# Optimization experiments

Hardware: AMD Instinct MI355X
Metric: run time of the kernel (lower is better)

The kernel has to match this reference:

```python
import jax, jax.numpy as jnp
import numpy as np

TOP_K = 8
NUM_EXPERTS = 64
TEMPERATURE = 1.0
ALPHA = 0.01
EPS = 1e-20


def setup_inputs() -> dict:
    key = jax.random.key(0)
    k1, k2 = jax.random.split(key)
    hidden_states = jax.random.normal(k1, (4, 8192, 1024), dtype=jnp.float32)
    # kaiming_uniform-ish scale for the router weight
    bound = 1.0 / np.sqrt(1024.0)
    weight = jax.random.uniform(k2, (NUM_EXPERTS, 1024), dtype=jnp.float32,
                                minval=-bound, maxval=bound)
    return {"hidden_states": hidden_states, "weight": weight}


def reference(hidden_states, weight):
    bsz, seq_len, hidden_dim = hidden_states.shape
    flat = hidden_states.reshape(-1, hidden_dim)            # [N, H], N = bsz*seq_len
    logits = jnp.einsum('nh,eh->ne', flat, weight) / TEMPERATURE  # [N, E]
    scores = jax.nn.softmax(logits, axis=-1)                # [N, E]
    topk_weight, topk_idx = jax.lax.top_k(scores, TOP_K)    # [N, k] each
    # renormalize top-k probabilities
    topk_weight = topk_weight / (topk_weight.sum(axis=-1, keepdims=True) + EPS)
    # aux load-balancing loss (seq_aux=False branch), scores detached
    scores_aux = jax.lax.stop_gradient(scores)
    idx_flat = topk_idx.reshape(-1)                         # [N*k]
    ce = jnp.zeros((NUM_EXPERTS,), dtype=jnp.float32).at[idx_flat].add(1.0)
    ce = ce / idx_flat.shape[0]                             # mean of one-hot rows
    pi = scores_aux.mean(axis=0)                            # [E]
    fi = ce * NUM_EXPERTS
    aux_loss = (pi * fi).sum() * ALPHA
    return topk_idx, topk_weight, aux_loss
```

## Files before the change

### kernel.cpp

```cpp
#include <hip/hip_runtime.h>

#define H 1024
#define E 64
#define BT 64
#define THETA 2e-4f

typedef __attribute__((ext_vector_type(4))) float f4;
typedef __attribute__((ext_vector_type(16))) float f32x16;
typedef __bf16 bf16x8 __attribute__((ext_vector_type(8)));
typedef unsigned int u32;
typedef __attribute__((ext_vector_type(4))) u32 u32x4;

__device__ __forceinline__ u32 cvtpk_bf16(float a, float b) {
    u32 r;
    asm("v_cvt_pk_bf16_f32 %0, %1, %2" : "=v"(r) : "v"(a), "v"(b));
    return r;
}
__device__ __forceinline__ float asfloat(u32 u) { union { u32 u; float f; } c; c.u = u; return c.f; }

__device__ __forceinline__ void split8(f4 a, f4 b, u32x4& hi, u32x4& lo) {
    float x0[4] = {a.x, a.z, b.x, b.z};
    float x1[4] = {a.y, a.w, b.y, b.w};
    #pragma unroll
    for (int i = 0; i < 4; ++i) {
        u32 h = cvtpk_bf16(x0[i], x1[i]);
        float r0 = x0[i] - asfloat(h << 16);
        float r1 = x1[i] - asfloat(h & 0xFFFF0000u);
        hi[i] = h;
        lo[i] = cvtpk_bf16(r0, r1);
    }
}

__device__ __forceinline__ void async16(const void* g, void* l) {
    __builtin_amdgcn_global_load_lds(
        (const __attribute__((address_space(1))) unsigned int*)g,
        (__attribute__((address_space(3))) unsigned int*)l,
        16, 0, 0);
}

__global__ __launch_bounds__(512, 4)
void gate_main(const float* __restrict__ hs, const float* __restrict__ wt,
               float* __restrict__ out, float* __restrict__ pi_ws,
               float* __restrict__ ce_ws, unsigned int* __restrict__ risk_cnt,
               unsigned int* __restrict__ risk_list, unsigned int risk_cap,
               int n_tokens) {
    __shared__ float smem[16384];
    const int t = threadIdx.x;
    const int wave = t >> 6, lane = t & 63;
    const int tok_base = blockIdx.x * BT;
    char* sb = (char*)smem;

    const int srow = t >> 3;
    const int srcj = (t & 7) ^ (srow & 7);
    const float* gA = hs + (size_t)(tok_base + srow) * H + srcj * 4;
    const float* gB = wt + (size_t)srow * H + srcj * 4;
    const int sdest = wave << 10;

    const int lr = lane & 31, kh = lane >> 5;
    const int q4 = wave & 3, kh2 = wave >> 2;
    const int wrow = (q4 >> 1) * 32;
    const int wcol = (q4 & 1) * 32;
    const int arow = wrow + lr, brow = wcol + lr;
    const int s0 = kh2 * 4 + kh * 2;
    const int aoff = arow * 128 + ((s0 ^ (arow & 7)) << 4);
    const int boff = 8192 + brow * 128 + ((s0 ^ (brow & 7)) << 4);

    f32x16 acc0, acc1;
    #pragma unroll
    for (int i = 0; i < 16; ++i) { acc0[i] = 0.f; acc1[i] = 0.f; }

    auto stage = [&](int c) {
        char* bb = sb + (c & 3) * 16384;
        async16(gA + c * 32, bb + sdest);
        async16(gB + c * 32, bb + 8192 + sdest);
    };
    auto compute = [&](int c) {
        const char* cb = sb + (c & 3) * 16384;
        f4 a0 = *(const f4*)(cb + aoff);
        f4 a1 = *(const f4*)(cb + (aoff ^ 16));
        f4 b0 = *(const f4*)(cb + boff);
        f4 b1 = *(const f4*)(cb + (boff ^ 16));
        u32x4 ahp, alp, bhp, blp;
        split8(a0, a1, ahp, alp);
        split8(b0, b1, bhp, blp);
        const bf16x8 ah = __builtin_bit_cast(bf16x8, ahp);
        const bf16x8 al = __builtin_bit_cast(bf16x8, alp);
        const bf16x8 bh = __builtin_bit_cast(bf16x8, bhp);
        const bf16x8 bl = __builtin_bit_cast(bf16x8, blp);
        acc0 = __builtin_amdgcn_mfma_f32_32x32x16_bf16(ah, bh, acc0, 0, 0, 0);
        acc1 = __builtin_amdgcn_mfma_f32_32x32x16_bf16(ah, bl, acc1, 0, 0, 0);
        acc1 = __builtin_amdgcn_mfma_f32_32x32x16_bf16(al, bh, acc1, 0, 0, 0);
    };

    stage(0); stage(1); stage(2);
    for (int c = 0; c < 30; ++c) {
        asm volatile("s_waitcnt vmcnt(4)" ::: "memory");
        __builtin_amdgcn_s_barrier();
        __builtin_amdgcn_sched_barrier(0);
        if (c < 29) stage(c + 3);
        __builtin_amdgcn_sched_barrier(0);
        compute(c);
    }
    asm volatile("s_waitcnt vmcnt(2)" ::: "memory");
    __builtin_amdgcn_s_barrier();
    __builtin_amdgcn_sched_barrier(0);
    compute(30);
    asm volatile("s_waitcnt vmcnt(0)" ::: "memory");
    __builtin_amdgcn_s_barrier();
    __builtin_amdgcn_sched_barrier(0);
    compute(31);
    __syncthreads();

    float* S = smem;
    f4* S4 = (f4*)smem;
    float* P2    = smem + 4352;
    float* recip = smem + 8448;
    float* hist  = smem + 8512;
    float* pi7   = smem + 8576;

    {
        float vs[16];
        #pragma unroll
        for (int i = 0; i < 16; ++i) vs[i] = acc0[i] + acc1[i];
        if (kh2) {
            #pragma unroll
            for (int gq = 0; gq < 4; ++gq)
                #pragma unroll
                for (int qq = 0; qq < 4; ++qq)
                    P2[q4 * 1024 + (qq + gq * 8 + kh * 4) * 32 + lr] = vs[gq * 4 + qq];
        }
        if (t < 64) hist[t] = 0.f;
        __syncthreads();
        if (!kh2) {
            #pragma unroll
            for (int gq = 0; gq < 4; ++gq)
                #pragma unroll
                for (int qq = 0; qq < 4; ++qq) {
                    const int row = qq + gq * 8 + kh * 4;
                    S[(wrow + row) * 68 + wcol + lr] =
                        vs[gq * 4 + qq] + P2[q4 * 1024 + row * 32 + lr];
                }
        }
    }
    __syncthreads();

    if (t < 256) {
        const int tok = t >> 2, q = t & 3;
        f4 v[4];
        #pragma unroll
        for (int c2 = 0; c2 < 4; ++c2) v[c2] = S4[tok * 17 + q * 4 + c2];
        float m = v[0].x;
        #pragma unroll
        for (int c2 = 0; c2 < 4; ++c2)
            m = fmaxf(m, fmaxf(fmaxf(v[c2].x, v[c2].y), fmaxf(v[c2].z, v[c2].w)));
        m = fmaxf(m, __shfl_xor(m, 1, 64));
        m = fmaxf(m, __shfl_xor(m, 2, 64));
        float lsum = 0.f;
        #pragma unroll
        for (int c2 = 0; c2 < 4; ++c2) {
            v[c2].x = __expf(v[c2].x - m); v[c2].y = __expf(v[c2].y - m);
            v[c2].z = __expf(v[c2].z - m); v[c2].w = __expf(v[c2].w - m);
            lsum += (v[c2].x + v[c2].y) + (v[c2].z + v[c2].w);
        }
        #pragma unroll
        for (int c2 = 0; c2 < 4; ++c2) S4[tok * 17 + q * 4 + c2] = v[c2];
        lsum += __shfl_xor(lsum, 1, 64);
        lsum += __shfl_xor(lsum, 2, 64);
        if (q == 0) recip[tok] = 1.0f / lsum;
    }
    __syncthreads();

    const int selw = blockIdx.x & 7;
    if (wave == selw) {
        const int tok = lane;
        const int tok_g = tok_base + tok;
        float val[9]; int idx[9];
        #pragma unroll
        for (int r = 0; r < 9; ++r) { val[r] = -1.f; idx[r] = 0; }
        #pragma unroll
        for (int c2 = 0; c2 < 16; ++c2) {
            f4 v = S4[tok * 17 + c2];
            float e4[4] = {v.x, v.y, v.z, v.w};
            #pragma unroll
            for (int u = 0; u < 4; ++u) {
                float cv = e4[u]; int ci = c2 * 4 + u;
                #pragma unroll
                for (int r = 0; r < 9; ++r) {
                    const bool g = cv > val[r];
                    const float tv = val[r]; const int ti = idx[r];
                    val[r] = g ? cv : tv;  idx[r] = g ? ci : ti;
                    cv = g ? tv : cv;      ci = g ? ti : ci;
                }
            }
        }
        const float s8 = ((val[0] + val[1]) + (val[2] + val[3]))
                       + ((val[4] + val[5]) + (val[6] + val[7]));
        const float wsum = s8 + 1e-20f;
        f4* out4 = (f4*)out;
        f4 o;
        o.x = (float)idx[0]; o.y = (float)idx[1]; o.z = (float)idx[2]; o.w = (float)idx[3];
        out4[(size_t)tok_g * 2] = o;
        o.x = (float)idx[4]; o.y = (float)idx[5]; o.z = (float)idx[6]; o.w = (float)idx[7];
        out4[(size_t)tok_g * 2 + 1] = o;
        const size_t wb = (size_t)n_tokens * 2;
        o.x = val[0] / wsum; o.y = val[1] / wsum; o.z = val[2] / wsum; o.w = val[3] / wsum;
        out4[wb + (size_t)tok_g * 2] = o;
        o.x = val[4] / wsum; o.y = val[5] / wsum; o.z = val[6] / wsum; o.w = val[7] / wsum;
        out4[wb + (size_t)tok_g * 2 + 1] = o;
        #pragma unroll
        for (int r = 0; r < 8; ++r) atomicAdd(&hist[idx[r]], 1.0f);
        float ming = 1e30f;
        #pragma unroll
        for (int r = 0; r < 8; ++r)
            ming = fminf(ming, (val[r] - val[r + 1]) / fmaxf(val[r], 1e-30f));
        if (ming < THETA) {
            unsigned int pos = atomicAdd(risk_cnt, 1u);
            if (pos < risk_cap) risk_list[pos] = (unsigned int)tok_g;
        }
    } else {
        const int sev = ((wave - selw) & 7) - 1;
        const int e = lane;
        const int t0 = sev * 9;
        const int t1 = (sev == 6) ? 64 : (t0 + 9);
        float part = 0.f;
        for (int tok = t0; tok < t1; ++tok)
            part = fmaf(S[tok * 68 + e], recip[tok], part);
        pi7[sev * 64 + e] = part;
    }
    __syncthreads();
    const int rep = (blockIdx.x & 7) << 6;
    if (t < 64) {
        const float p = ((pi7[t] + pi7[64 + t]) + (pi7[128 + t] + pi7[192 + t]))
                      + ((pi7[256 + t] + pi7[320 + t]) + pi7[384 + t]);
        atomicAdd(&pi_ws[rep + t], p);
    } else if (t < 128) {
        atomicAdd(&ce_ws[rep + (t - 64)], hist[t - 64]);
    }
}

__global__ __launch_bounds__(256)
void gate_fixup(const float* __restrict__ hs, const float* __restrict__ wt,
                float* __restrict__ out, const unsigned int* __restrict__ risk_cnt,
                const unsigned int* __restrict__ risk_list, unsigned int risk_cap,
                int n_tokens, const float* __restrict__ pi_ws,
                const float* __restrict__ ce_ws) {
    __shared__ float hrow[H];
    __shared__ double red[256];
    const int t = threadIdx.x;

    if (blockIdx.x == 0 && t < 64) {
        double pi = 0.0, ce = 0.0;
        #pragma unroll
        for (int rp = 0; rp < 8; ++rp) {
            pi += (double)pi_ws[rp * 64 + t];
            ce += (double)ce_ws[rp * 64 + t];
        }
        pi /= (double)n_tokens;
        ce /= ((double)n_tokens * 8.0);
        double term = pi * ce * 64.0;
        #pragma unroll
        for (int off = 32; off > 0; off >>= 1) term += __shfl_xor(term, off, 64);
        if (t == 0) out[(size_t)n_tokens * 16] = (float)(term * 0.01);
    }

    unsigned int cnt = *risk_cnt;
    if (cnt > risk_cap) cnt = risk_cap;

    for (unsigned int u = blockIdx.x; u < cnt; u += gridDim.x) {
        const int tok = (int)risk_list[u];
        ((float4*)hrow)[t] = ((const float4*)(hs + (size_t)tok * H))[t];
        __syncthreads();

        const int e = t >> 2, sl = t & 3;
        const float4* wp = (const float4*)wt + (size_t)e * 256;
        const float4* hp = (const float4*)hrow;
        double acc = 0.0;
        #pragma unroll 8
        for (int k4 = 0; k4 < 64; ++k4) {
            float4 wv = wp[k4 * 4 + sl];
            float4 hv = hp[k4 * 4 + sl];
            acc = fma((double)wv.x, (double)hv.x, acc);
            acc = fma((double)wv.y, (double)hv.y, acc);
            acc = fma((double)wv.z, (double)hv.z, acc);
            acc = fma((double)wv.w, (double)hv.w, acc);
        }
        red[t] = acc;
        __syncthreads();

        if (t < 64) {
            const int lane = t;
            double lg = red[t * 4] + red[t * 4 + 1] + red[t * 4 + 2] + red[t * 4 + 3];
            double m = lg;
            #pragma unroll
            for (int off = 32; off > 0; off >>= 1) {
                double o = __shfl_xor(m, off, 64);
                m = (o > m) ? o : m;
            }
            const double p = exp(lg - m);
            double v = lg, psum = 0.0, mypv = 0.0;
            int myidx = 0;
            for (int r = 0; r < 8; ++r) {
                double bv = v; int bi = lane;
                #pragma unroll
                for (int off = 32; off > 0; off >>= 1) {
                    double ov = __shfl_xor(bv, off, 64);
                    int    oi = __shfl_xor(bi, off, 64);
                    if (ov > bv || (ov == bv && oi < bi)) { bv = ov; bi = oi; }
                }
                double pw = __shfl(p, bi, 64);
                psum += pw;
                if (lane == r) { myidx = bi; mypv = pw; }
                if (lane == bi) v = -1e300;
            }
            const double wsum = psum + 1e-20;
            if (lane < 8) {
                out[(size_t)tok * 8 + lane] = (float)myidx;
                out[(size_t)n_tokens * 8 + (size_t)tok * 8 + lane] = (float)(mypv / wsum);
            }
        }
        __syncthreads();
    }
}

extern "C" void kernel_launch(void* const* d_in, const int* in_sizes, int n_in,
                              void* d_out, int out_size, void* d_ws, size_t ws_size,
                              hipStream_t stream) {
    const float* hs = (const float*)d_in[0];
    const float* wt = (const float*)d_in[1];
    float* out = (float*)d_out;
    const int n_tokens = in_sizes[0] / H;

    float* pi_ws = (float*)d_ws;
    float* ce_ws = (float*)((char*)d_ws + 2048);
    unsigned int* risk_cnt  = (unsigned int*)((char*)d_ws + 4096);
    unsigned int* risk_list = (unsigned int*)((char*)d_ws + 4608);
    unsigned int risk_cap = (unsigned int)((ws_size > 4608 ? (ws_size - 4608) : 0) / 4);
    if (risk_cap > (unsigned int)n_tokens) risk_cap = (unsigned int)n_tokens;

    size_t zbytes = ws_size < 4608 ? ws_size : 4608;
    hipMemsetAsync(d_ws, 0, zbytes, stream);

    gate_main<<<n_tokens / BT, 512, 0, stream>>>(hs, wt, out, pi_ws, ce_ws,
                                                 risk_cnt, risk_list, risk_cap, n_tokens);
    gate_fixup<<<256, 256, 0, stream>>>(hs, wt, out, risk_cnt, risk_list, risk_cap,
                                        n_tokens, pi_ws, ce_ws);
}
```

Measured before the change: 238.5 us.

## Give each wave private LDS staging to drop block barriers from GEMM loop

Replaces the shared 4-stage block-wide LDS ring with per-wave private double buffers. Each wave now loads exactly the A and B fragments it consumes, so the per-chunk s_barrier is no longer needed. This removes block-level synchronisation in the main loop. In exchange, the shared rows are loaded redundantly by different waves, the pipeline depth shrinks, and the loads no longer use the swizzled coalesced pattern. It also lowers THETA, the threshold for flagging near-tie tokens onto the risk list for the fallback pass.

```diff
diff --git a/kernel.cpp b/kernel.cpp
--- a/kernel.cpp
+++ b/kernel.cpp
@@ -3,7 +3,7 @@
 #define H 1024
 #define E 64
 #define BT 64
-#define THETA 2e-4f
+#define THETA 1e-4f
 
 typedef __attribute__((ext_vector_type(4))) float f4;
 typedef __attribute__((ext_vector_type(16))) float f32x16;
@@ -50,36 +50,45 @@
     const int tok_base = blockIdx.x * BT;
     char* sb = (char*)smem;
 
-    const int srow = t >> 3;
-    const int srcj = (t & 7) ^ (srow & 7);
-    const float* gA = hs + (size_t)(tok_base + srow) * H + srcj * 4;
-    const float* gB = wt + (size_t)srow * H + srcj * 4;
-    const int sdest = wave << 10;
-
     const int lr = lane & 31, kh = lane >> 5;
     const int q4 = wave & 3, kh2 = wave >> 2;
     const int wrow = (q4 >> 1) * 32;
     const int wcol = (q4 & 1) * 32;
-    const int arow = wrow + lr, brow = wcol + lr;
-    const int s0 = kh2 * 4 + kh * 2;
-    const int aoff = arow * 128 + ((s0 ^ (arow & 7)) << 4);
-    const int boff = 8192 + brow * 128 + ((s0 ^ (brow & 7)) << 4);
+
+    const float* pA0 = hs + (size_t)(tok_base + wrow + lr) * H + (kh2 * 4 + kh) * 4;
+    const float* pA1 = pA0 + 8;
+    const float* pB0 = wt + (size_t)(wcol + lr) * H + (kh2 * 4 + kh) * 4;
+    const float* pB1 = pB0 + 8;
+    char* wb = sb + wave * 8192;
+
+    const int ra = kh * 1024 + lr * 16;
+    const int rb = 2048 + ra;
 
     f32x16 acc0, acc1;
     #pragma unroll
     for (int i = 0; i < 16; ++i) { acc0[i] = 0.f; acc1[i] = 0.f; }
 
     auto stage = [&](int c) {
-        char* bb = sb + (c & 3) * 16384;
-        async16(gA + c * 32, bb + sdest);
-        async16(gB + c * 32, bb + 8192 + sdest);
+        char* bb = wb + (c & 1) * 4096;
+        async16(pA0 + c * 32, bb);
+        async16(pA1 + c * 32, bb + 1024);
+        async16(pB0 + c * 32, bb + 2048);
+        async16(pB1 + c * 32, bb + 3072);
     };
-    auto compute = [&](int c) {
-        const char* cb = sb + (c & 3) * 16384;
-        f4 a0 = *(const f4*)(cb + aoff);
-        f4 a1 = *(const f4*)(cb + (aoff ^ 16));
-        f4 b0 = *(const f4*)(cb + boff);
-        f4 b1 = *(const f4*)(cb + (boff ^ 16));
+
+    stage(0); stage(1);
+
+    for (int c = 0; c < 32; ++c) {
+        if (c < 31) { asm volatile("s_waitcnt vmcnt(4)" ::: "memory"); }
+        else        { asm volatile("s_waitcnt vmcnt(0)" ::: "memory"); }
+        __builtin_amdgcn_sched_barrier(0);
+        const char* bb = wb + (c & 1) * 4096;
+        f4 a0 = *(const f4*)(bb + ra);
+        f4 a1 = *(const f4*)(bb + ra + 512);
+        f4 b0 = *(const f4*)(bb + rb);
+        f4 b1 = *(const f4*)(bb + rb + 512);
+        __builtin_amdgcn_sched_barrier(0);
+        if (c + 2 < 32) stage(c + 2);
         u32x4 ahp, alp, bhp, blp;
         split8(a0, a1, ahp, alp);
         split8(b0, b1, bhp, blp);
@@ -90,25 +99,7 @@
         acc0 = __builtin_amdgcn_mfma_f32_32x32x16_bf16(ah, bh, acc0, 0, 0, 0);
         acc1 = __builtin_amdgcn_mfma_f32_32x32x16_bf16(ah, bl, acc1, 0, 0, 0);
         acc1 = __builtin_amdgcn_mfma_f32_32x32x16_bf16(al, bh, acc1, 0, 0, 0);
-    };
-
-    stage(0); stage(1); stage(2);
-    for (int c = 0; c < 30; ++c) {
-        asm volatile("s_waitcnt vmcnt(4)" ::: "memory");
-        __builtin_amdgcn_s_barrier();
-        __builtin_amdgcn_sched_barrier(0);
-        if (c < 29) stage(c + 3);
-        __builtin_amdgcn_sched_barrier(0);
-        compute(c);
-    }
-    asm volatile("s_waitcnt vmcnt(2)" ::: "memory");
-    __builtin_amdgcn_s_barrier();
-    __builtin_amdgcn_sched_barrier(0);
-    compute(30);
-    asm volatile("s_waitcnt vmcnt(0)" ::: "memory");
-    __builtin_amdgcn_s_barrier();
-    __builtin_amdgcn_sched_barrier(0);
-    compute(31);
+    }
     __syncthreads();
 
     float* S = smem;
@@ -202,11 +193,11 @@
         out4[(size_t)tok_g * 2] = o;
         o.x = (float)idx[4]; o.y = (float)idx[5]; o.z = (float)idx[6]; o.w = (float)idx[7];
         out4[(size_t)tok_g * 2 + 1] = o;
-        const size_t wb = (size_t)n_tokens * 2;
+        const size_t wb2 = (size_t)n_tokens * 2;
         o.x = val[0] / wsum; o.y = val[1] / wsum; o.z = val[2] / wsum; o.w = val[3] / wsum;
-        out4[wb + (size_t)tok_g * 2] = o;
+        out4[wb2 + (size_t)tok_g * 2] = o;
         o.x = val[4] / wsum; o.y = val[5] / wsum; o.z = val[6] / wsum; o.w = val[7] / wsum;
-        out4[wb + (size_t)tok_g * 2 + 1] = o;
+        out4[wb2 + (size_t)tok_g * 2 + 1] = o;
         #pragma unroll
         for (int r = 0; r < 8; ++r) atomicAdd(&hist[idx[r]], 1.0f);
         float ming = 1e30f;
```

Measured after the change: 270.0 us. +13.2%, slower.
